# Kernel optimization log

Measured on AMD Instinct MI355X. Metric: run time of the kernel, lower is better.

## Reference

```python
import jax, jax.numpy as jnp
import numpy as np

B, T, H = 64, 256, 128

def setup_inputs() -> dict:
    key = jax.random.key(0)
    ks = jax.random.split(key, 10)
    s = 1.0 / np.sqrt(H)
    return {
        "x": jax.random.normal(ks[0], (B, T, 2), jnp.float32),
        "enc_output": jax.random.normal(ks[1], (B, T, H), jnp.float32),
        "h0": jax.random.normal(ks[2], (B, H), jnp.float32) * s,
        "c0": jax.random.normal(ks[3], (B, H), jnp.float32) * s,
        "W1": jax.random.normal(ks[4], (H, H), jnp.float32) * s,
        "W2": jax.random.normal(ks[5], (H, H), jnp.float32) * s,
        "V": jax.random.normal(ks[6], (H,), jnp.float32) * s,
        "Wk": jax.random.normal(ks[7], (2, 4 * H), jnp.float32) * (1.0 / np.sqrt(2.0)),
        "Wr": jax.random.normal(ks[8], (H, 4 * H), jnp.float32) * s,
        "b": jnp.zeros((4 * H,), jnp.float32),
    }


def reference(x, enc_output, h0, c0, W1, W2, V, Wk, Wr, b):
    Bb, Tt, _ = x.shape
    # Precompute W1 @ enc_output once (original recomputes it T times inside K.rnn)
    enc_proj = jnp.einsum('bth,hk->btk', enc_output, W1)  # [B,T,H]

    def lstm_cell(inp, h, c):
        # Keras LSTMCell, gate order i,f,c,o; sigmoid recurrent activation, tanh activation
        z = inp @ Wk + h @ Wr + b  # [B,4H]
        zi, zf, zg, zo = jnp.split(z, 4, axis=-1)
        i = jax.nn.sigmoid(zi)
        f = jax.nn.sigmoid(zf)
        g = jnp.tanh(zg)
        o = jax.nn.sigmoid(zo)
        c_new = f * c + i * g
        h_new = o * jnp.tanh(c_new)
        return h_new, c_new

    def step(carry, _):
        h, c, ptr = carry
        h, c = lstm_cell(ptr, h, c)
        # additive attention over all encoder steps, batched (replaces inner K.rnn)
        scores = jnp.einsum('btk,k->bt', jnp.tanh(enc_proj + (h @ W2)[:, None, :]), V)
        probs = jax.nn.softmax(scores, axis=1)  # [B,T]
        # get_pointer with rank=0: top-1 of descending argsort == argmax
        idx = jnp.argmax(probs, axis=1)  # [B]
        ptr = jnp.take_along_axis(x, idx[:, None, None], axis=1)[:, 0, :]  # [B,2]
        return (h, c, ptr), probs

    ptr0 = jnp.ones((Bb, 2), x.dtype)
    _, probs_seq = jax.lax.scan(step, (h0, c0, ptr0), None, length=Tt)  # [T,B,T]
    return jnp.transpose(probs_seq, (1, 0, 2))  # [B,T,T]
```

## Files before the change

kernel.cpp:

```cpp
#include <hip/hip_runtime.h>
#include <cstddef>

#define TT 256
#define HH 128
#define EST 132
#define SCPS 260

__device__ __forceinline__ float rdlane(float v, int l) {
  return __int_as_float(__builtin_amdgcn_readlane(__float_as_int(v), l));
}
__device__ __forceinline__ float fast_sigmoid(float x) {
  const float L2E = 1.4426950408889634f;
  float y = __builtin_amdgcn_exp2f(-x * L2E);
  return __builtin_amdgcn_rcpf(1.0f + y);
}
__device__ __forceinline__ float fast_tanh(float x) {
  const float C2 = 2.8853900817779268f;
  float y = __builtin_amdgcn_exp2f(x * C2);
  return 1.0f - 2.0f * __builtin_amdgcn_rcpf(1.0f + y);
}

__global__ __launch_bounds__(512, 2)
void decoder_kernel(const float* __restrict__ x,
                    const float* __restrict__ enc_output,
                    const float* __restrict__ h0,
                    const float* __restrict__ c0,
                    const float* __restrict__ W1,
                    const float* __restrict__ W2,
                    const float* __restrict__ V,
                    const float* __restrict__ Wk,
                    const float* __restrict__ Wr,
                    const float* __restrict__ bias,
                    float* __restrict__ out)
{
  __shared__ float E[TT * EST];
  __shared__ float zpart[4 * 512];
  __shared__ float scp[8 * SCPS];
  __shared__ float hbuf[HH];
  __shared__ float xloc[TT * 2];

  const int u    = threadIdx.x;
  const int b    = blockIdx.x;
  const int lane = u & 63;
  const int w    = u >> 6;
  const float C2  = 2.8853900817779268f;
  const float L2E = 1.4426950408889634f;

  {
    const float* encb = enc_output + (size_t)b * TT * HH;
    const int tsub = u >> 4;
    const int ks   = (u & 15) * 8;
    for (int p = 0; p < 8; ++p) {
      const int tt = p * 32 + tsub;
      float4 a0 = {0.f, 0.f, 0.f, 0.f};
      float4 a1 = {0.f, 0.f, 0.f, 0.f};
      const float4* er4 = (const float4*)(encb + tt * HH);
      for (int j4 = 0; j4 < 32; ++j4) {
        const float4 ev = er4[j4];
        const float* w1p = W1 + (j4 * 4) * HH + ks;
        float4 wa, wb;
        wa = *(const float4*)(w1p + 0 * HH); wb = *(const float4*)(w1p + 0 * HH + 4);
        a0.x += ev.x * wa.x; a0.y += ev.x * wa.y; a0.z += ev.x * wa.z; a0.w += ev.x * wa.w;
        a1.x += ev.x * wb.x; a1.y += ev.x * wb.y; a1.z += ev.x * wb.z; a1.w += ev.x * wb.w;
        wa = *(const float4*)(w1p + 1 * HH); wb = *(const float4*)(w1p + 1 * HH + 4);
        a0.x += ev.y * wa.x; a0.y += ev.y * wa.y; a0.z += ev.y * wa.z; a0.w += ev.y * wa.w;
        a1.x += ev.y * wb.x; a1.y += ev.y * wb.y; a1.z += ev.y * wb.z; a1.w += ev.y * wb.w;
        wa = *(const float4*)(w1p + 2 * HH); wb = *(const float4*)(w1p + 2 * HH + 4);
        a0.x += ev.z * wa.x; a0.y += ev.z * wa.y; a0.z += ev.z * wa.z; a0.w += ev.z * wa.w;
        a1.x += ev.z * wb.x; a1.y += ev.z * wb.y; a1.z += ev.z * wb.z; a1.w += ev.z * wb.w;
        wa = *(const float4*)(w1p + 3 * HH); wb = *(const float4*)(w1p + 3 * HH + 4);
        a0.x += ev.w * wa.x; a0.y += ev.w * wa.y; a0.z += ev.w * wa.z; a0.w += ev.w * wa.w;
        a1.x += ev.w * wb.x; a1.y += ev.w * wb.y; a1.z += ev.w * wb.z; a1.w += ev.w * wb.w;
      }
      *(float4*)(&E[tt * EST + ks])     = a0;
      *(float4*)(&E[tt * EST + ks + 4]) = a1;
    }
  }
  xloc[u] = x[b * (TT * 2) + u];

  const int kq = u >> 7;
  const int cs = u & 127;
  float4 wr4[32];
  #pragma unroll
  for (int i = 0; i < 32; ++i)
    wr4[i] = *(const float4*)(Wr + (32 * kq + i) * 512 + 4 * cs);
  const int m = 32 * (w & 3) + (lane & 31);
  float wkA[4], wkB[4], bbg[4];
  #pragma unroll
  for (int gg = 0; gg < 4; ++gg) {
    wkA[gg] = Wk[gg * HH + m];
    wkB[gg] = Wk[512 + gg * HH + m];
    bbg[gg] = bias[gg * HH + m];
  }
  float c = c0[b * HH + m];
  const int kk = lane & 15;
  const int jq = lane >> 4;
  float w2local[32];
  #pragma unroll
  for (int i = 0; i < 32; ++i)
    w2local[i] = W2[(32 * jq + i) * HH + 16 * w + kk];
  const float v2r = -2.0f * V[16 * w + kk];
  float vL[16];
  #pragma unroll
  for (int i = 0; i < 16; ++i) vL[i] = rdlane(v2r, i);
  float ptr0 = 1.0f, ptr1 = 1.0f;
  float svr;
  {
    float v = V[lane] + V[64 + lane];
    #pragma unroll
    for (int o = 1; o < 64; o <<= 1) v += __shfl_xor(v, o, 64);
    svr = v;
  }

  __syncthreads();

  {
    float* Er = &E[(u >> 1) * EST + 64 * (u & 1)];
    #pragma unroll
    for (int i = 0; i < 16; ++i) {
      float4 ev = *(const float4*)(Er + 4 * i);
      ev.x = __builtin_amdgcn_exp2f(ev.x * C2);
      ev.y = __builtin_amdgcn_exp2f(ev.y * C2);
      ev.z = __builtin_amdgcn_exp2f(ev.z * C2);
      ev.w = __builtin_amdgcn_exp2f(ev.w * C2);
      *(float4*)(Er + 4 * i) = ev;
    }
  }
  {
    float hA0 = h0[(size_t)b * HH + 32 * kq + (lane & 31)];
    float4 zac = {0.f, 0.f, 0.f, 0.f};
    #pragma unroll
    for (int i = 0; i < 32; ++i) {
      float hi = rdlane(hA0, i);
      zac.x += hi * wr4[i].x;
      zac.y += hi * wr4[i].y;
      zac.z += hi * wr4[i].z;
      zac.w += hi * wr4[i].w;
    }
    *(float4*)(&zpart[kq * 512 + 4 * cs]) = zac;
  }
  __syncthreads();

  float* outb = out + (size_t)b * TT * TT;

  #pragma unroll 1
  for (int step = 0; step < TT; ++step) {
    if (step > 0 && w < 4) {
      float4 sc = {0.f, 0.f, 0.f, 0.f};
      #pragma unroll
      for (int q = 0; q < 8; ++q) {
        float4 v = *(const float4*)(&scp[q * SCPS + 4 * lane]);
        sc.x += v.x; sc.y += v.y; sc.z += v.z; sc.w += v.w;
      }
      sc.x += svr; sc.y += svr; sc.z += svr; sc.w += svr;
      float p0 = __builtin_amdgcn_exp2f((sc.x - 12.0f) * L2E);
      float p1 = __builtin_amdgcn_exp2f((sc.y - 12.0f) * L2E);
      float p2 = __builtin_amdgcn_exp2f((sc.z - 12.0f) * L2E);
      float p3 = __builtin_amdgcn_exp2f((sc.w - 12.0f) * L2E);
      float m4 = fmaxf(fmaxf(sc.x, sc.y), fmaxf(sc.z, sc.w));
      int ttl = (sc.x == m4) ? 0 : (sc.y == m4) ? 1 : (sc.z == m4) ? 2 : 3;
      float ws4 = (p0 + p1) + (p2 + p3);
      float mx = m4;
      #pragma unroll
      for (int o = 1; o < 64; o <<= 1) {
        mx  = fmaxf(mx, __shfl_xor(mx, o));
        ws4 += __shfl_xor(ws4, o);
      }
      unsigned long long bal = __ballot(m4 == mx);
      int ls  = __ffsll(bal) - 1;
      int tc  = 4 * lane + ttl;
      int tts = __builtin_amdgcn_readlane(tc, ls);
      ptr0 = xloc[2 * tts + 0];
      ptr1 = xloc[2 * tts + 1];
      if ((lane >> 4) == w) {
        float rs = __builtin_amdgcn_rcpf(ws4);
        float4 po = {p0 * rs, p1 * rs, p2 * rs, p3 * rs};
        *(float4*)(&outb[(size_t)(step - 1) * TT + 4 * lane]) = po;
      }
    }
    if ((lane & 32) == 0 && w < 4) {
      float z0 = bbg[0] + ptr0 * wkA[0] + ptr1 * wkB[0];
      float z1 = bbg[1] + ptr0 * wkA[1] + ptr1 * wkB[1];
      float z2 = bbg[2] + ptr0 * wkA[2] + ptr1 * wkB[2];
      float z3 = bbg[3] + ptr0 * wkA[3] + ptr1 * wkB[3];
      #pragma unroll
      for (int q = 0; q < 4; ++q) {
        z0 += zpart[q * 512 + 0 * HH + m];
        z1 += zpart[q * 512 + 1 * HH + m];
        z2 += zpart[q * 512 + 2 * HH + m];
        z3 += zpart[q * 512 + 3 * HH + m];
      }
      float ig = fast_sigmoid(z0);
      float fg = fast_sigmoid(z1);
      float gg = fast_tanh(z2);
      float og = fast_sigmoid(z3);
      c = fg * c + ig * gg;
      hbuf[m] = og * fast_tanh(c);
    }
    __syncthreads();

    float Uk;
    {
      float cp0 = 0.0f, cp1 = 0.0f;
      const float4* h4 = (const float4*)(hbuf + 32 * jq);
      #pragma unroll
      for (int i4 = 0; i4 < 8; ++i4) {
        float4 hv = h4[i4];
        cp0 += hv.x * w2local[4 * i4 + 0];
        cp1 += hv.y * w2local[4 * i4 + 1];
        cp0 += hv.z * w2local[4 * i4 + 2];
        cp1 += hv.w * w2local[4 * i4 + 3];
      }
      float csum = cp0 + cp1;
      csum += __shfl_xor(csum, 16);
      csum += __shfl_xor(csum, 32);
      Uk = __builtin_amdgcn_exp2f(csum * C2);
    }
    {
      float uL[16];
      #pragma unroll
      for (int i = 0; i < 16; ++i) uL[i] = rdlane(Uk, i);
      #pragma unroll
      for (int tt = 0; tt < 4; ++tt) {
        const float* Er = &E[(64 * tt + lane) * EST + 16 * w];
        float4 e0 = *(const float4*)(Er + 0);
        float4 e1 = *(const float4*)(Er + 4);
        float4 e2 = *(const float4*)(Er + 8);
        float4 e3 = *(const float4*)(Er + 12);
        float a0 = 0.0f, a1 = 0.0f;
        float t0, t1, n;
        t0 = fmaf(e0.x, uL[ 0], 1.0f); t1 = fmaf(e0.y, uL[ 1], 1.0f);
        n  = fmaf(vL[ 1], t0, vL[ 0] * t1);
        a0 = fmaf(n, __builtin_amdgcn_rcpf(t0 * t1), a0);
        t0 = fmaf(e0.z, uL[ 2], 1.0f); t1 = fmaf(e0.w, uL[ 3], 1.0f);
        n  = fmaf(vL[ 3], t0, vL[ 2] * t1);
        a1 = fmaf(n, __builtin_amdgcn_rcpf(t0 * t1), a1);
        t0 = fmaf(e1.x, uL[ 4], 1.0f); t1 = fmaf(e1.y, uL[ 5], 1.0f);
        n  = fmaf(vL[ 5], t0, vL[ 4] * t1);
        a0 = fmaf(n, __builtin_amdgcn_rcpf(t0 * t1), a0);
        t0 = fmaf(e1.z, uL[ 6], 1.0f); t1 = fmaf(e1.w, uL[ 7], 1.0f);
        n  = fmaf(vL[ 7], t0, vL[ 6] * t1);
        a1 = fmaf(n, __builtin_amdgcn_rcpf(t0 * t1), a1);
        t0 = fmaf(e2.x, uL[ 8], 1.0f); t1 = fmaf(e2.y, uL[ 9], 1.0f);
        n  = fmaf(vL[ 9], t0, vL[ 8] * t1);
        a0 = fmaf(n, __builtin_amdgcn_rcpf(t0 * t1), a0);
        t0 = fmaf(e2.z, uL[10], 1.0f); t1 = fmaf(e2.w, uL[11], 1.0f);
        n  = fmaf(vL[11], t0, vL[10] * t1);
        a1 = fmaf(n, __builtin_amdgcn_rcpf(t0 * t1), a1);
        t0 = fmaf(e3.x, uL[12], 1.0f); t1 = fmaf(e3.y, uL[13], 1.0f);
        n  = fmaf(vL[13], t0, vL[12] * t1);
        a0 = fmaf(n, __builtin_amdgcn_rcpf(t0 * t1), a0);
        t0 = fmaf(e3.z, uL[14], 1.0f); t1 = fmaf(e3.w, uL[15], 1.0f);
        n  = fmaf(vL[15], t0, vL[14] * t1);
        a1 = fmaf(n, __builtin_amdgcn_rcpf(t0 * t1), a1);
        scp[w * SCPS + 64 * tt + lane] = a0 + a1;
      }
    }
    {
      float hA = hbuf[32 * kq + (lane & 31)];
      float4 zac = {0.f, 0.f, 0.f, 0.f};
      #pragma unroll
      for (int i = 0; i < 32; ++i) {
        float hi = rdlane(hA, i);
        zac.x += hi * wr4[i].x;
        zac.y += hi * wr4[i].y;
        zac.z += hi * wr4[i].z;
        zac.w += hi * wr4[i].w;
      }
      *(float4*)(&zpart[kq * 512 + 4 * cs]) = zac;
    }
    __syncthreads();
  }

  if (w < 4) {
    float4 sc = {0.f, 0.f, 0.f, 0.f};
    #pragma unroll
    for (int q = 0; q < 8; ++q) {
      float4 v = *(const float4*)(&scp[q * SCPS + 4 * lane]);
      sc.x += v.x; sc.y += v.y; sc.z += v.z; sc.w += v.w;
    }
    sc.x += svr; sc.y += svr; sc.z += svr; sc.w += svr;
    float p0 = __builtin_amdgcn_exp2f((sc.x - 12.0f) * L2E);
    float p1 = __builtin_amdgcn_exp2f((sc.y - 12.0f) * L2E);
    float p2 = __builtin_amdgcn_exp2f((sc.z - 12.0f) * L2E);
    float p3 = __builtin_amdgcn_exp2f((sc.w - 12.0f) * L2E);
    float ws4 = (p0 + p1) + (p2 + p3);
    #pragma unroll
    for (int o = 1; o < 64; o <<= 1) ws4 += __shfl_xor(ws4, o);
    if ((lane >> 4) == w) {
      float rs = __builtin_amdgcn_rcpf(ws4);
      float4 po = {p0 * rs, p1 * rs, p2 * rs, p3 * rs};
      *(float4*)(&outb[(size_t)255 * TT + 4 * lane]) = po;
    }
  }
}

extern "C" void kernel_launch(void* const* d_in, const int* in_sizes, int n_in,
                              void* d_out, int out_size, void* d_ws, size_t ws_size,
                              hipStream_t stream) {
  (void)in_sizes; (void)n_in; (void)d_ws; (void)ws_size; (void)out_size;
  const float* x    = (const float*)d_in[0];
  const float* enc  = (const float*)d_in[1];
  const float* h0   = (const float*)d_in[2];
  const float* c0   = (const float*)d_in[3];
  const float* W1   = (const float*)d_in[4];
  const float* W2   = (const float*)d_in[5];
  const float* V    = (const float*)d_in[6];
  const float* Wk   = (const float*)d_in[7];
  const float* Wr   = (const float*)d_in[8];
  const float* bias = (const float*)d_in[9];
  float* out = (float*)d_out;

  decoder_kernel<<<64, 512, 0, stream>>>(x, enc, h0, c0, W1, W2, V, Wk, Wr, bias, out);
}
```

Before: 833.2 us.

## Split softmax and argmax across wave groups, keep x in registers

```diff
diff --git a/kernel.cpp b/kernel.cpp
--- a/kernel.cpp
+++ b/kernel.cpp
@@ -37,7 +37,6 @@
   __shared__ float zpart[4 * 512];
   __shared__ float scp[8 * SCPS];
   __shared__ float hbuf[HH];
-  __shared__ float xloc[TT * 2];
 
   const int u    = threadIdx.x;
   const int b    = blockIdx.x;
@@ -76,7 +75,6 @@
       *(float4*)(&E[tt * EST + ks + 4]) = a1;
     }
   }
-  xloc[u] = x[b * (TT * 2) + u];
 
   const int kq = u >> 7;
   const int cs = u & 127;
@@ -93,6 +91,10 @@
     bbg[gg] = bias[gg * HH + m];
   }
   float c = c0[b * HH + m];
+  float2 xr0 = *(const float2*)(x + b * (TT * 2) + 2 * (0 * 64 + lane));
+  float2 xr1 = *(const float2*)(x + b * (TT * 2) + 2 * (1 * 64 + lane));
+  float2 xr2 = *(const float2*)(x + b * (TT * 2) + 2 * (2 * 64 + lane));
+  float2 xr3 = *(const float2*)(x + b * (TT * 2) + 2 * (3 * 64 + lane));
   const int kk = lane & 15;
   const int jq = lane >> 4;
   float w2local[32];
@@ -145,37 +147,42 @@
 
   #pragma unroll 1
   for (int step = 0; step < TT; ++step) {
-    if (step > 0 && w < 4) {
+    if (step > 0) {
       float4 sc = {0.f, 0.f, 0.f, 0.f};
       #pragma unroll
       for (int q = 0; q < 8; ++q) {
         float4 v = *(const float4*)(&scp[q * SCPS + 4 * lane]);
         sc.x += v.x; sc.y += v.y; sc.z += v.z; sc.w += v.w;
       }
-      sc.x += svr; sc.y += svr; sc.z += svr; sc.w += svr;
-      float p0 = __builtin_amdgcn_exp2f((sc.x - 12.0f) * L2E);
-      float p1 = __builtin_amdgcn_exp2f((sc.y - 12.0f) * L2E);
-      float p2 = __builtin_amdgcn_exp2f((sc.z - 12.0f) * L2E);
-      float p3 = __builtin_amdgcn_exp2f((sc.w - 12.0f) * L2E);
-      float m4 = fmaxf(fmaxf(sc.x, sc.y), fmaxf(sc.z, sc.w));
-      int ttl = (sc.x == m4) ? 0 : (sc.y == m4) ? 1 : (sc.z == m4) ? 2 : 3;
-      float ws4 = (p0 + p1) + (p2 + p3);
-      float mx = m4;
-      #pragma unroll
-      for (int o = 1; o < 64; o <<= 1) {
-        mx  = fmaxf(mx, __shfl_xor(mx, o));
-        ws4 += __shfl_xor(ws4, o);
-      }
-      unsigned long long bal = __ballot(m4 == mx);
-      int ls  = __ffsll(bal) - 1;
-      int tc  = 4 * lane + ttl;
-      int tts = __builtin_amdgcn_readlane(tc, ls);
-      ptr0 = xloc[2 * tts + 0];
-      ptr1 = xloc[2 * tts + 1];
-      if ((lane >> 4) == w) {
-        float rs = __builtin_amdgcn_rcpf(ws4);
-        float4 po = {p0 * rs, p1 * rs, p2 * rs, p3 * rs};
-        *(float4*)(&outb[(size_t)(step - 1) * TT + 4 * lane]) = po;
+      if (w < 4) {
+        float m4 = fmaxf(fmaxf(sc.x, sc.y), fmaxf(sc.z, sc.w));
+        int ttl = (sc.x == m4) ? 0 : (sc.y == m4) ? 1 : (sc.z == m4) ? 2 : 3;
+        float mx = m4;
+        #pragma unroll
+        for (int o = 1; o < 64; o <<= 1) mx = fmaxf(mx, __shfl_xor(mx, o));
+        unsigned long long bal = __ballot(m4 == mx);
+        int ls  = __ffsll(bal) - 1;
+        int tc  = 4 * lane + ttl;
+        int tts = __builtin_amdgcn_readlane(tc, ls);
+        int j   = tts >> 6;
+        int ll  = tts & 63;
+        float2 cand = (j == 0) ? xr0 : (j == 1) ? xr1 : (j == 2) ? xr2 : xr3;
+        ptr0 = rdlane(cand.x, ll);
+        ptr1 = rdlane(cand.y, ll);
+      } else {
+        sc.x += svr; sc.y += svr; sc.z += svr; sc.w += svr;
+        float p0 = __builtin_amdgcn_exp2f((sc.x - 12.0f) * L2E);
+        float p1 = __builtin_amdgcn_exp2f((sc.y - 12.0f) * L2E);
+        float p2 = __builtin_amdgcn_exp2f((sc.z - 12.0f) * L2E);
+        float p3 = __builtin_amdgcn_exp2f((sc.w - 12.0f) * L2E);
+        float ws4 = (p0 + p1) + (p2 + p3);
+        #pragma unroll
+        for (int o = 1; o < 64; o <<= 1) ws4 += __shfl_xor(ws4, o);
+        if ((lane >> 4) == (w - 4)) {
+          float rs = __builtin_amdgcn_rcpf(ws4);
+          float4 po = {p0 * rs, p1 * rs, p2 * rs, p3 * rs};
+          *(float4*)(&outb[(size_t)(step - 1) * TT + 4 * lane]) = po;
+        }
       }
     }
     if ((lane & 32) == 0 && w < 4) {
@@ -257,22 +264,34 @@
       }
     }
     {
-      float hA = hbuf[32 * kq + (lane & 31)];
+      const float4* h4 = (const float4*)(hbuf + 32 * kq);
       float4 zac = {0.f, 0.f, 0.f, 0.f};
       #pragma unroll
-      for (int i = 0; i < 32; ++i) {
-        float hi = rdlane(hA, i);
-        zac.x += hi * wr4[i].x;
-        zac.y += hi * wr4[i].y;
-        zac.z += hi * wr4[i].z;
-        zac.w += hi * wr4[i].w;
+      for (int i4 = 0; i4 < 8; ++i4) {
+        float4 hv = h4[i4];
+        zac.x += hv.x * wr4[4 * i4 + 0].x;
+        zac.y += hv.x * wr4[4 * i4 + 0].y;
+        zac.z += hv.x * wr4[4 * i4 + 0].z;
+        zac.w += hv.x * wr4[4 * i4 + 0].w;
+        zac.x += hv.y * wr4[4 * i4 + 1].x;
+        zac.y += hv.y * wr4[4 * i4 + 1].y;
+        zac.z += hv.y * wr4[4 * i4 + 1].z;
+        zac.w += hv.y * wr4[4 * i4 + 1].w;
+        zac.x += hv.z * wr4[4 * i4 + 2].x;
+        zac.y += hv.z * wr4[4 * i4 + 2].y;
+        zac.z += hv.z * wr4[4 * i4 + 2].z;
+        zac.w += hv.z * wr4[4 * i4 + 2].w;
+        zac.x += hv.w * wr4[4 * i4 + 3].x;
+        zac.y += hv.w * wr4[4 * i4 + 3].y;
+        zac.z += hv.w * wr4[4 * i4 + 3].z;
+        zac.w += hv.w * wr4[4 * i4 + 3].w;
       }
       *(float4*)(&zpart[kq * 512 + 4 * cs]) = zac;
     }
     __syncthreads();
   }
 
-  if (w < 4) {
+  if (w >= 4) {
     float4 sc = {0.f, 0.f, 0.f, 0.f};
     #pragma unroll
     for (int q = 0; q < 8; ++q) {
@@ -287,7 +306,7 @@
     float ws4 = (p0 + p1) + (p2 + p3);
     #pragma unroll
     for (int o = 1; o < 64; o <<= 1) ws4 += __shfl_xor(ws4, o);
-    if ((lane >> 4) == w) {
+    if ((lane >> 4) == (w - 4)) {
       float rs = __builtin_amdgcn_rcpf(ws4);
       float4 po = {p0 * rs, p1 * rs, p2 * rs, p3 * rs};
       *(float4*)(&outb[(size_t)255 * TT + 4 * lane]) = po;
```

New measurement: 809.4 us. -2.9%, faster.
